# Performance work log

Hardware: AMD Instinct MI355X
Metric: run time of the kernel (lower is better)

## Reference

```python
import jax, jax.numpy as jnp
import numpy as np

N = 50000
IN_CH = 256
HID = 16
HEADS = 4
OUT_CH = 40
E = 800000
NEG_SLOPE = 0.2


def gat_layer(x, src, dst, W, a_src, a_dst, b, heads, out_ch, concat):
    n = x.shape[0]
    h = (x @ W).reshape(n, heads, out_ch)               # [N, H, C]
    al_src = jnp.einsum('nhc,hc->nh', h, a_src)          # [N, H]
    al_dst = jnp.einsum('nhc,hc->nh', h, a_dst)
    e = jax.nn.leaky_relu(al_src[src] + al_dst[dst], NEG_SLOPE)  # [E, H]
    m = jax.ops.segment_max(e, dst, num_segments=n)      # per-dst max for stability
    e = jnp.exp(e - m[dst])
    denom = jax.ops.segment_sum(e, dst, num_segments=n)
    alpha = e / (denom[dst] + 1e-16)                     # segment softmax [E, H]
    msg = h[src] * alpha[:, :, None]                     # [E, H, C]
    out = jax.ops.segment_sum(msg, dst, num_segments=n)  # [N, H, C]
    out = out.reshape(n, heads * out_ch) if concat else out.mean(axis=1)
    return out + b


def setup_inputs() -> dict:
    key = jax.random.key(0)
    ks = jax.random.split(key, 10)
    glorot = lambda k, shape: jax.random.normal(k, shape, jnp.float32) * np.sqrt(2.0 / (shape[0] + shape[-1]))
    return {
        'x': jax.random.normal(ks[0], (N, IN_CH), jnp.float32),
        'edge_index': jax.random.randint(ks[1], (2, E), 0, N, jnp.int64),
        'W1': glorot(ks[2], (IN_CH, HEADS * HID)),
        'a_src1': glorot(ks[3], (HEADS, HID)),
        'a_dst1': glorot(ks[4], (HEADS, HID)),
        'b1': jnp.zeros((HEADS * HID,), jnp.float32),
        'W2': glorot(ks[5], (HEADS * HID, OUT_CH)),
        'a_src2': glorot(ks[6], (1, OUT_CH)),
        'a_dst2': glorot(ks[7], (1, OUT_CH)),
        'b2': jnp.zeros((OUT_CH,), jnp.float32),
    }


def reference(x, edge_index, W1, a_src1, a_dst1, b1, W2, a_src2, a_dst2, b2):
    n = x.shape[0]
    loops = jnp.arange(n, dtype=edge_index.dtype)
    src = jnp.concatenate([edge_index[0], loops])  # PyG GATConv adds self-loops
    dst = jnp.concatenate([edge_index[1], loops])
    h = gat_layer(x, src, dst, W1, a_src1, a_dst1, b1, HEADS, HID, concat=True)
    h = jax.nn.elu(h)
    out = gat_layer(h, src, dst, W2, a_src2, a_dst2, b2, 1, OUT_CH, concat=False)
    return jax.nn.log_softmax(out, axis=-1)
```

## Files before the change

### kernel.cpp

```cpp
#include <hip/hip_runtime.h>
#include <math.h>

static constexpr int IN_CH  = 256;
static constexpr int HD1    = 64;
static constexpr int HEADS  = 4;
static constexpr int OUT_CH = 40;
static constexpr float NEG  = 0.2f;
static constexpr int BSH    = 7;
static constexpr int BRNG   = 128;

typedef __attribute__((ext_vector_type(8))) short bf16x8;
typedef __attribute__((ext_vector_type(4))) short s16x4;
typedef __attribute__((ext_vector_type(4))) float f32x4;

static __device__ __forceinline__ short f2bf(float f) {
    union { float f; unsigned u; } v; v.f = f;
    unsigned r = v.u + 0x7FFFu + ((v.u >> 16) & 1u);
    return (short)(r >> 16);
}
static __device__ __forceinline__ float bf2f(unsigned short u) {
    union { unsigned u; float f; } v; v.u = ((unsigned)u) << 16;
    return v.f;
}

__global__ __launch_bounds__(256) void k_bhist(const int* __restrict__ dst, int* __restrict__ bcnt,
                                               int E, int B, int perBlk) {
    __shared__ int lcnt[4096];
    for (int i = threadIdx.x; i < B; i += 256) lcnt[i] = 0;
    __syncthreads();
    const int s0 = blockIdx.x * perBlk;
    const int s1 = min(s0 + perBlk, E);
    for (int i = s0 + threadIdx.x; i < s1; i += 256)
        atomicAdd(&lcnt[dst[i] >> BSH], 1);
    __syncthreads();
    for (int i = threadIdx.x; i < B; i += 256)
        if (lcnt[i]) atomicAdd(&bcnt[i], lcnt[i]);
}

__global__ __launch_bounds__(256) void k_balloc(const int* __restrict__ bcnt, int* __restrict__ ebstart,
        int* __restrict__ ebcur, int* __restrict__ sstart, int* __restrict__ totals, int B, int n) {
    int t = blockIdx.x * 256 + threadIdx.x;
    if (t < B) {
        int ec = bcnt[t];
        int nodes = min(n - (t << BSH), BRNG);
        ebstart[t] = atomicAdd(&totals[0], ec);
        ebcur[t]   = ebstart[t];
        sstart[t]  = atomicAdd(&totals[1], ec + nodes);
    }
}

__global__ __launch_bounds__(256) void k_bpart(const int* __restrict__ ei, int* __restrict__ ebcur,
        uint2* __restrict__ ebuf, int E, int B, int perBlk) {
    __shared__ int lcnt[4096];
    __shared__ int lofs[4096];
    for (int i = threadIdx.x; i < B; i += 256) lcnt[i] = 0;
    __syncthreads();
    const int s0 = blockIdx.x * perBlk;
    const int s1 = min(s0 + perBlk, E);
    for (int i = s0 + threadIdx.x; i < s1; i += 256)
        atomicAdd(&lcnt[ei[E + i] >> BSH], 1);
    __syncthreads();
    for (int i = threadIdx.x; i < B; i += 256) {
        const int c = lcnt[i];
        lofs[i] = c ? atomicAdd(&ebcur[i], c) : 0;
        lcnt[i] = 0;
    }
    __syncthreads();
    for (int i = s0 + threadIdx.x; i < s1; i += 256) {
        const int d = ei[E + i], s = ei[i];
        const int b = d >> BSH;
        const int r = atomicAdd(&lcnt[b], 1);
        ebuf[lofs[b] + r] = make_uint2((unsigned)s, (unsigned)d);
    }
}

__global__ __launch_bounds__(256) void k_bcsr(const uint2* __restrict__ ebuf,
        const int* __restrict__ ebstart, const int* __restrict__ bcnt, const int* __restrict__ sstart,
        int* __restrict__ rowstart, int* __restrict__ counts, int* __restrict__ ssrc, int n) {
    __shared__ int ncnt[BRNG], rloc[BRNG], cur[BRNG];
    const int b = blockIdx.x;
    const int t = threadIdx.x;
    const int n0 = b << BSH;
    const int nodes = min(n - n0, BRNG);
    const int ec = bcnt[b];
    const int e0 = ebstart[b];
    const int s0 = sstart[b];

    if (t < BRNG) ncnt[t] = (t < nodes) ? 1 : 0;
    __syncthreads();
    for (int i = t; i < ec; i += 256)
        atomicAdd(&ncnt[ebuf[e0 + i].y & (BRNG - 1)], 1);
    __syncthreads();

    if (t < BRNG) rloc[t] = ncnt[t];
    __syncthreads();
    #pragma unroll
    for (int off = 1; off < BRNG; off <<= 1) {
        int u = 0;
        if (t < BRNG && t >= off) u = rloc[t - off];
        __syncthreads();
        if (t < BRNG) rloc[t] += u;
        __syncthreads();
    }

    if (t < nodes) {
        const int ex = rloc[t] - ncnt[t];
        rowstart[n0 + t] = s0 + ex;
        counts[n0 + t]   = ncnt[t];
        ssrc[s0 + ex]    = n0 + t;
        cur[t] = ex + 1;
    }
    __syncthreads();
    for (int i = t; i < ec; i += 256) {
        const uint2 e = ebuf[e0 + i];
        const int lo = (int)e.y & (BRNG - 1);
        const int p = atomicAdd(&cur[lo], 1);
        ssrc[s0 + p] = (int)e.x;
    }
}

__global__ __launch_bounds__(256) void k_xform1(const float* __restrict__ x,
        const float* __restrict__ W1, const float* __restrict__ a_src, const float* __restrict__ a_dst,
        unsigned short* __restrict__ h1b, float* __restrict__ alsrc, float* __restrict__ aldst, int n)
{
    __shared__ short W1T[64][264];
    const int t = threadIdx.x;
    const int l = t & 63;
    const int w = t >> 6;

    {
        const int c = l;
        #pragma unroll
        for (int i = 0; i < 16; ++i) {
            const int kb = i * 16 + w * 4;
            s16x4 pk;
            pk[0] = f2bf(W1[(kb + 0) * 64 + c]);
            pk[1] = f2bf(W1[(kb + 1) * 64 + c]);
            pk[2] = f2bf(W1[(kb + 2) * 64 + c]);
            pk[3] = f2bf(W1[(kb + 3) * 64 + c]);
            *(s16x4*)&W1T[c][kb] = pk;
        }
    }
    __syncthreads();

    const int r0 = blockIdx.x * 64 + w * 16;
    const int lr = l & 15;
    const int lk = l >> 4;

    f32x4 acc[4];
    #pragma unroll
    for (int ct = 0; ct < 4; ++ct) acc[ct] = (f32x4){0.f, 0.f, 0.f, 0.f};

    int rowA = r0 + lr; if (rowA > n - 1) rowA = n - 1;
    const float* xrow = x + (size_t)rowA * IN_CH + lk * 8;

    float4 a0 = *(const float4*)(xrow);
    float4 a1 = *(const float4*)(xrow + 4);

    for (int ks = 0; ks < 8; ++ks) {
        bf16x8 bfrag[4];
        #pragma unroll
        for (int ct = 0; ct < 4; ++ct)
            bfrag[ct] = *(const bf16x8*)&W1T[ct * 16 + lr][ks * 32 + lk * 8];

        const float4 c0 = a0, c1 = a1;
        if (ks < 7) {
            a0 = *(const float4*)(xrow + (ks + 1) * 32);
            a1 = *(const float4*)(xrow + (ks + 1) * 32 + 4);
        }
        bf16x8 afrag;
        afrag[0] = f2bf(c0.x); afrag[1] = f2bf(c0.y);
        afrag[2] = f2bf(c0.z); afrag[3] = f2bf(c0.w);
        afrag[4] = f2bf(c1.x); afrag[5] = f2bf(c1.y);
        afrag[6] = f2bf(c1.z); afrag[7] = f2bf(c1.w);

        #pragma unroll
        for (int ct = 0; ct < 4; ++ct)
            acc[ct] = __builtin_amdgcn_mfma_f32_16x16x32_bf16(afrag, bfrag[ct], acc[ct], 0, 0, 0);
    }

    #pragma unroll
    for (int ct = 0; ct < 4; ++ct) {
        #pragma unroll
        for (int reg = 0; reg < 4; ++reg) {
            const int row = r0 + lk * 4 + reg;
            if (row < n) h1b[(size_t)row * HD1 + ct * 16 + lr] = (unsigned short)f2bf(acc[ct][reg]);
        }
    }

    float asv[4], adv[4];
    #pragma unroll
    for (int ct = 0; ct < 4; ++ct) { asv[ct] = a_src[ct * 16 + lr]; adv[ct] = a_dst[ct * 16 + lr]; }

    #pragma unroll
    for (int reg = 0; reg < 4; ++reg) {
        const int row = r0 + lk * 4 + reg;
        #pragma unroll
        for (int ct = 0; ct < 4; ++ct) {
            float s1 = acc[ct][reg] * asv[ct];
            float s2 = acc[ct][reg] * adv[ct];
            s1 += __shfl_xor(s1, 1); s1 += __shfl_xor(s1, 2);
            s1 += __shfl_xor(s1, 4); s1 += __shfl_xor(s1, 8);
            s2 += __shfl_xor(s2, 1); s2 += __shfl_xor(s2, 2);
            s2 += __shfl_xor(s2, 4); s2 += __shfl_xor(s2, 8);
            if (lr == 0 && row < n) {
                alsrc[row * HEADS + ct] = s1;
                aldst[row * HEADS + ct] = s2;
            }
        }
    }
}

__global__ __launch_bounds__(256) void k_aggr1(const unsigned short* __restrict__ h1b,
        const float* __restrict__ alsrc, const float* __restrict__ aldst, const float* __restrict__ b1,
        const int* __restrict__ rowstart, const int* __restrict__ counts, const int* __restrict__ ssrc,
        float* __restrict__ hact, int n)
{
    const int wid  = (blockIdx.x * blockDim.x + threadIdx.x) >> 6;
    const int lane = threadIdx.x & 63;
    const int sub  = lane & 15;
    const int head = sub >> 2;

    int nid = wid * 4 + (lane >> 4);
    const bool valid = nid < n;
    if (!valid) nid = n - 1;

    const int rs  = rowstart[nid];
    const int cnt = valid ? counts[nid] : 0;

    int maxcnt = cnt;
    maxcnt = max(maxcnt, __shfl_xor(maxcnt, 16));
    maxcnt = max(maxcnt, __shfl_xor(maxcnt, 32));

    float m = -1e30f;
    {
        const float adA = aldst[nid * HEADS + (sub & 3)];
        const int npairs = cnt * 4, maxpairs = maxcnt * 4;
        for (int idx = sub; idx < maxpairs; idx += 16) {
            if (idx < npairs) {
                int s = ssrc[rs + (idx >> 2)];
                float l = alsrc[s * HEADS + (sub & 3)] + adA;
                l = l > 0.f ? l : NEG * l;
                m = fmaxf(m, l);
            }
        }
        #pragma unroll
        for (int off = 1; off < 16; off <<= 1) m = fmaxf(m, __shfl_xor(m, off));
    }

    const float adB = aldst[nid * HEADS + head];
    float d = 0.f;
    float4 acc = make_float4(0.f, 0.f, 0.f, 0.f);
    for (int i0 = 0; i0 < maxcnt; i0 += 4) {
        int  sv[4]; bool on[4];
        #pragma unroll
        for (int u = 0; u < 4; ++u) {
            const int i = i0 + u;
            on[u] = i < cnt;
            sv[u] = on[u] ? ssrc[rs + i] : 0;
        }
        ushort4 hv[4]; float lv[4];
        #pragma unroll
        for (int u = 0; u < 4; ++u) {
            hv[u] = *(const ushort4*)(h1b + (size_t)sv[u] * HD1 + sub * 4);
            lv[u] = alsrc[sv[u] * HEADS + head];
        }
        #pragma unroll
        for (int u = 0; u < 4; ++u) {
            float l = lv[u] + adB;
            l = l > 0.f ? l : NEG * l;
            const float p = on[u] ? __expf(l - m) : 0.f;
            d += p;
            acc.x = fmaf(p, bf2f(hv[u].x), acc.x);
            acc.y = fmaf(p, bf2f(hv[u].y), acc.y);
            acc.z = fmaf(p, bf2f(hv[u].z), acc.z);
            acc.w = fmaf(p, bf2f(hv[u].w), acc.w);
        }
    }

    const float inv = 1.f / (d + 1e-16f);
    const float4 bv = *(const float4*)(b1 + sub * 4);
    float4 v;
    v.x = acc.x * inv + bv.x;  v.y = acc.y * inv + bv.y;
    v.z = acc.z * inv + bv.z;  v.w = acc.w * inv + bv.w;
    v.x = v.x > 0.f ? v.x : __expf(v.x) - 1.f;
    v.y = v.y > 0.f ? v.y : __expf(v.y) - 1.f;
    v.z = v.z > 0.f ? v.z : __expf(v.z) - 1.f;
    v.w = v.w > 0.f ? v.w : __expf(v.w) - 1.f;
    if (valid) *(float4*)(hact + (size_t)nid * HD1 + sub * 4) = v;
}

__global__ __launch_bounds__(64) void k_xform2(const float* __restrict__ hin,
        const float* __restrict__ W2, const float* __restrict__ a_src, const float* __restrict__ a_dst,
        unsigned short* __restrict__ h2b, float* __restrict__ alsrc, float* __restrict__ aldst, int n)
{
    __shared__ float Ws[HD1 * OUT_CH];
    const int t = threadIdx.x;
    #pragma unroll
    for (int i = 0; i < 10; ++i) ((float4*)Ws)[i * 64 + t] = ((const float4*)W2)[i * 64 + t];
    __syncthreads();

    const int r = blockIdx.x * 64 + t;
    if (r >= n) return;

    float acc[OUT_CH];
    #pragma unroll
    for (int j = 0; j < OUT_CH; ++j) acc[j] = 0.f;

    const float4* hr = (const float4*)(hin + (size_t)r * HD1);
    for (int kq = 0; kq < 16; ++kq) {
        const float4 xv = hr[kq];
        #pragma unroll
        for (int kk = 0; kk < 4; ++kk) {
            const float xs = (kk == 0) ? xv.x : (kk == 1) ? xv.y : (kk == 2) ? xv.z : xv.w;
            const float* wrow = Ws + (kq * 4 + kk) * OUT_CH;
            #pragma unroll
            for (int jq = 0; jq < 10; ++jq) {
                const float4 w = *(const float4*)(wrow + jq * 4);
                acc[jq * 4 + 0] = fmaf(xs, w.x, acc[jq * 4 + 0]);
                acc[jq * 4 + 1] = fmaf(xs, w.y, acc[jq * 4 + 1]);
                acc[jq * 4 + 2] = fmaf(xs, w.z, acc[jq * 4 + 2]);
                acc[jq * 4 + 3] = fmaf(xs, w.w, acc[jq * 4 + 3]);
            }
        }
    }

    float s1 = 0.f, s2 = 0.f;
    #pragma unroll
    for (int jq = 0; jq < 10; ++jq) {
        const float4 av = ((const float4*)a_src)[jq];
        const float4 dv = ((const float4*)a_dst)[jq];
        s1 += acc[jq*4+0] * av.x + acc[jq*4+1] * av.y + acc[jq*4+2] * av.z + acc[jq*4+3] * av.w;
        s2 += acc[jq*4+0] * dv.x + acc[jq*4+1] * dv.y + acc[jq*4+2] * dv.z + acc[jq*4+3] * dv.w;
        ushort4 pk;
        pk.x = (unsigned short)f2bf(acc[jq*4+0]);
        pk.y = (unsigned short)f2bf(acc[jq*4+1]);
        pk.z = (unsigned short)f2bf(acc[jq*4+2]);
        pk.w = (unsigned short)f2bf(acc[jq*4+3]);
        *(ushort4*)(h2b + (size_t)r * OUT_CH + jq * 4) = pk;
    }
    alsrc[r] = s1;
    aldst[r] = s2;
}

__global__ __launch_bounds__(256) void k_aggr2(const unsigned short* __restrict__ h2b,
        const float* __restrict__ alsrc, const float* __restrict__ aldst, const float* __restrict__ b2,
        const int* __restrict__ rowstart, const int* __restrict__ counts, const int* __restrict__ ssrc,
        float* __restrict__ out, int n)
{
    const int wid  = (blockIdx.x * blockDim.x + threadIdx.x) >> 6;
    const int lane = threadIdx.x & 63;
    const int sub  = lane & 15;
    const bool act = sub < 10;
    const int subc = act ? sub : 0;

    int nid = wid * 4 + (lane >> 4);
    const bool valid = nid < n;
    if (!valid) nid = n - 1;

    const int rs  = rowstart[nid];
    const int cnt = valid ? counts[nid] : 0;

    int maxcnt = cnt;
    maxcnt = max(maxcnt, __shfl_xor(maxcnt, 16));
    maxcnt = max(maxcnt, __shfl_xor(maxcnt, 32));

    const float ad = aldst[nid];

    float m = -1e30f;
    for (int e = sub; e < maxcnt; e += 16) {
        if (e < cnt) {
            int s = ssrc[rs + e];
            float l = alsrc[s] + ad;
            l = l > 0.f ? l : NEG * l;
            m = fmaxf(m, l);
        }
    }
    #pragma unroll
    for (int off = 1; off < 16; off <<= 1) m = fmaxf(m, __shfl_xor(m, off));

    float d = 0.f;
    float4 acc = make_float4(0.f, 0.f, 0.f, 0.f);
    for (int i0 = 0; i0 < maxcnt; i0 += 4) {
        int  sv[4]; bool on[4];
        #pragma unroll
        for (int u = 0; u < 4; ++u) {
            const int i = i0 + u;
            on[u] = i < cnt;
            sv[u] = on[u] ? ssrc[rs + i] : 0;
        }
        ushort4 hv[4]; float lv[4];
        #pragma unroll
        for (int u = 0; u < 4; ++u) {
            hv[u] = *(const ushort4*)(h2b + (size_t)sv[u] * OUT_CH + subc * 4);
            lv[u] = alsrc[sv[u]];
        }
        #pragma unroll
        for (int u = 0; u < 4; ++u) {
            float l = lv[u] + ad;
            l = l > 0.f ? l : NEG * l;
            const float p = on[u] ? __expf(l - m) : 0.f;
            d += p;
            acc.x = fmaf(p, bf2f(hv[u].x), acc.x);
            acc.y = fmaf(p, bf2f(hv[u].y), acc.y);
            acc.z = fmaf(p, bf2f(hv[u].z), acc.z);
            acc.w = fmaf(p, bf2f(hv[u].w), acc.w);
        }
    }

    const float inv = 1.f / (d + 1e-16f);
    const float4 bv = *(const float4*)(b2 + subc * 4);
    float4 v;
    v.x = acc.x * inv + bv.x;  v.y = acc.y * inv + bv.y;
    v.z = acc.z * inv + bv.z;  v.w = acc.w * inv + bv.w;

    float mv = act ? fmaxf(fmaxf(v.x, v.y), fmaxf(v.z, v.w)) : -1e30f;
    #pragma unroll
    for (int off = 1; off < 16; off <<= 1) mv = fmaxf(mv, __shfl_xor(mv, off));
    float ex = act ? (__expf(v.x - mv) + __expf(v.y - mv) + __expf(v.z - mv) + __expf(v.w - mv)) : 0.f;
    #pragma unroll
    for (int off = 1; off < 16; off <<= 1) ex += __shfl_xor(ex, off);
    const float lse = mv + __logf(ex);

    if (valid && act) {
        *(float4*)(out + (size_t)nid * OUT_CH + sub * 4) =
            make_float4(v.x - lse, v.y - lse, v.z - lse, v.w - lse);
    }
}

extern "C" void kernel_launch(void* const* d_in, const int* in_sizes, int n_in,
                              void* d_out, int out_size, void* d_ws, size_t ws_size,
                              hipStream_t stream) {
    const float* x      = (const float*)d_in[0];
    const int*   ei     = (const int*)d_in[1];
    const float* W1     = (const float*)d_in[2];
    const float* a_src1 = (const float*)d_in[3];
    const float* a_dst1 = (const float*)d_in[4];
    const float* b1     = (const float*)d_in[5];
    const float* W2     = (const float*)d_in[6];
    const float* a_src2 = (const float*)d_in[7];
    const float* a_dst2 = (const float*)d_in[8];
    const float* b2     = (const float*)d_in[9];
    float* out = (float*)d_out;

    const int N = in_sizes[0] / IN_CH;
    const int E = in_sizes[1] / 2;
    const int B = (N + BRNG - 1) >> BSH;

    char* p = (char*)d_ws;
    auto alloc = [&](size_t bytes) -> void* {
        void* r = (void*)p;
        p += (bytes + 255) & ~(size_t)255;
        return r;
    };
    int*   counts   = (int*)alloc((size_t)N * 4);
    int*   rowstart = (int*)alloc((size_t)N * 4);
    int*   ssrc     = (int*)alloc((size_t)(E + N) * 4);
    int*   bmeta    = (int*)alloc((size_t)(B + 2) * 4);
    int*   ebstart  = (int*)alloc((size_t)B * 4);
    int*   ebcur    = (int*)alloc((size_t)B * 4);
    int*   sstart   = (int*)alloc((size_t)B * 4);
    unsigned short* h1b = (unsigned short*)alloc((size_t)N * HD1 * 2);
    unsigned short* h2b = (unsigned short*)alloc((size_t)N * OUT_CH * 2);
    float* alsrc1   = (float*)alloc((size_t)N * HEADS * 4);
    float* aldst1   = (float*)alloc((size_t)N * HEADS * 4);
    float* hact     = (float*)alloc((size_t)N * HD1 * 4);
    uint2* ebuf     = (uint2*)hact;
    int* bcnt   = bmeta;
    int* totals = bmeta + B;
    float* alsrc2 = alsrc1; float* aldst2 = aldst1;

    const int perBlk = 8192;
    const int nblkE  = (E + perBlk - 1) / perBlk;
    const int nblk64 = (N + 63) / 64;
    const int nblkAg = (N + 15) / 16;

    hipMemsetAsync(bmeta, 0, (size_t)(B + 2) * 4, stream);
    k_bhist <<<nblkE, 256, 0, stream>>>(ei + E, bcnt, E, B, perBlk);
    k_balloc<<<(B + 255) / 256, 256, 0, stream>>>(bcnt, ebstart, ebcur, sstart, totals, B, N);
    k_bpart <<<nblkE, 256, 0, stream>>>(ei, ebcur, ebuf, E, B, perBlk);
    k_bcsr  <<<B, 256, 0, stream>>>(ebuf, ebstart, bcnt, sstart, rowstart, counts, ssrc, N);

    k_xform1 <<<nblk64, 256, 0, stream>>>(x, W1, a_src1, a_dst1, h1b, alsrc1, aldst1, N);
    k_aggr1  <<<nblkAg, 256, 0, stream>>>(h1b, alsrc1, aldst1, b1, rowstart, counts, ssrc, hact, N);
    k_xform2 <<<nblk64, 64, 0, stream>>>(hact, W2, a_src2, a_dst2, h2b, alsrc2, aldst2, N);
    k_aggr2  <<<nblkAg, 256, 0, stream>>>(h2b, alsrc2, aldst2, b2, rowstart, counts, ssrc, out, N);
}
```

Before: 148.9 us.

## Replace per-node softmax max pass with global max-based upper bound

Both aggregation kernels stop doing a separate pass over each node's edges to find the per-destination max logit. Instead, the transform kernels reduce a global max of the source attention scores per head (via ordered-uint atomicMax), and the aggregation uses leaky_relu(dst score + global max) as the stabilizer. This relies on softmax being shift-invariant and leaky_relu being monotonic, so it removes a full gather pass over edges. The risk is exp underflow when a node's true max is far below the bound. The hipMemsetAsync call is also replaced by a small zeroing kernel that also clears the max slots.

Result: slower. 160.7 us (+7.9%).

```diff
diff --git a/kernel.cpp b/kernel.cpp
--- a/kernel.cpp
+++ b/kernel.cpp
@@ -21,6 +21,20 @@
 static __device__ __forceinline__ float bf2f(unsigned short u) {
     union { unsigned u; float f; } v; v.u = ((unsigned)u) << 16;
     return v.f;
+}
+static __device__ __forceinline__ unsigned f2ord(float f) {
+    unsigned u = __float_as_uint(f);
+    return (u & 0x80000000u) ? ~u : (u | 0x80000000u);
+}
+static __device__ __forceinline__ float ord2f(unsigned k) {
+    unsigned u = (k & 0x80000000u) ? (k ^ 0x80000000u) : ~k;
+    return __uint_as_float(u);
+}
+
+__global__ __launch_bounds__(256) void k_zero(int* __restrict__ bmeta, unsigned* __restrict__ gmax, int B) {
+    int t = blockIdx.x * 256 + threadIdx.x;
+    if (t < B + 2) bmeta[t] = 0;
+    if (t < 8) gmax[t] = 0u;
 }
 
 __global__ __launch_bounds__(256) void k_bhist(const int* __restrict__ dst, int* __restrict__ bcnt,
@@ -121,9 +135,11 @@
 
 __global__ __launch_bounds__(256) void k_xform1(const float* __restrict__ x,
         const float* __restrict__ W1, const float* __restrict__ a_src, const float* __restrict__ a_dst,
-        unsigned short* __restrict__ h1b, float* __restrict__ alsrc, float* __restrict__ aldst, int n)
+        unsigned short* __restrict__ h1b, float* __restrict__ alsrc, float* __restrict__ aldst,
+        unsigned* __restrict__ gmax, int n)
 {
     __shared__ short W1T[64][264];
+    __shared__ float wmax[4][4];
     const int t = threadIdx.x;
     const int l = t & 63;
     const int w = t >> 6;
@@ -192,6 +208,7 @@
     #pragma unroll
     for (int ct = 0; ct < 4; ++ct) { asv[ct] = a_src[ct * 16 + lr]; adv[ct] = a_dst[ct * 16 + lr]; }
 
+    float mh[4] = {-1e30f, -1e30f, -1e30f, -1e30f};
     #pragma unroll
     for (int reg = 0; reg < 4; ++reg) {
         const int row = r0 + lk * 4 + reg;
@@ -203,18 +220,30 @@
             s1 += __shfl_xor(s1, 4); s1 += __shfl_xor(s1, 8);
             s2 += __shfl_xor(s2, 1); s2 += __shfl_xor(s2, 2);
             s2 += __shfl_xor(s2, 4); s2 += __shfl_xor(s2, 8);
+            mh[ct] = fmaxf(mh[ct], s1);
             if (lr == 0 && row < n) {
                 alsrc[row * HEADS + ct] = s1;
                 aldst[row * HEADS + ct] = s2;
             }
         }
     }
+    #pragma unroll
+    for (int ct = 0; ct < 4; ++ct) {
+        mh[ct] = fmaxf(mh[ct], __shfl_xor(mh[ct], 16));
+        mh[ct] = fmaxf(mh[ct], __shfl_xor(mh[ct], 32));
+    }
+    if (l == 0) { wmax[w][0] = mh[0]; wmax[w][1] = mh[1]; wmax[w][2] = mh[2]; wmax[w][3] = mh[3]; }
+    __syncthreads();
+    if (t < 4) {
+        float m = fmaxf(fmaxf(wmax[0][t], wmax[1][t]), fmaxf(wmax[2][t], wmax[3][t]));
+        atomicMax(&gmax[t], f2ord(m));
+    }
 }
 
 __global__ __launch_bounds__(256) void k_aggr1(const unsigned short* __restrict__ h1b,
         const float* __restrict__ alsrc, const float* __restrict__ aldst, const float* __restrict__ b1,
         const int* __restrict__ rowstart, const int* __restrict__ counts, const int* __restrict__ ssrc,
-        float* __restrict__ hact, int n)
+        const unsigned* __restrict__ gmax, float* __restrict__ hact, int n)
 {
     const int wid  = (blockIdx.x * blockDim.x + threadIdx.x) >> 6;
     const int lane = threadIdx.x & 63;
@@ -232,23 +261,10 @@
     maxcnt = max(maxcnt, __shfl_xor(maxcnt, 16));
     maxcnt = max(maxcnt, __shfl_xor(maxcnt, 32));
 
-    float m = -1e30f;
-    {
-        const float adA = aldst[nid * HEADS + (sub & 3)];
-        const int npairs = cnt * 4, maxpairs = maxcnt * 4;
-        for (int idx = sub; idx < maxpairs; idx += 16) {
-            if (idx < npairs) {
-                int s = ssrc[rs + (idx >> 2)];
-                float l = alsrc[s * HEADS + (sub & 3)] + adA;
-                l = l > 0.f ? l : NEG * l;
-                m = fmaxf(m, l);
-            }
-        }
-        #pragma unroll
-        for (int off = 1; off < 16; off <<= 1) m = fmaxf(m, __shfl_xor(m, off));
-    }
-
     const float adB = aldst[nid * HEADS + head];
+    float m = adB + ord2f(gmax[head]);
+    m = m > 0.f ? m : NEG * m;
+
     float d = 0.f;
     float4 acc = make_float4(0.f, 0.f, 0.f, 0.f);
     for (int i0 = 0; i0 < maxcnt; i0 += 4) {
@@ -292,7 +308,8 @@
 
 __global__ __launch_bounds__(64) void k_xform2(const float* __restrict__ hin,
         const float* __restrict__ W2, const float* __restrict__ a_src, const float* __restrict__ a_dst,
-        unsigned short* __restrict__ h2b, float* __restrict__ alsrc, float* __restrict__ aldst, int n)
+        unsigned short* __restrict__ h2b, float* __restrict__ alsrc, float* __restrict__ aldst,
+        unsigned* __restrict__ gmax, int n)
 {
     __shared__ float Ws[HD1 * OUT_CH];
     const int t = threadIdx.x;
@@ -300,8 +317,9 @@
     for (int i = 0; i < 10; ++i) ((float4*)Ws)[i * 64 + t] = ((const float4*)W2)[i * 64 + t];
     __syncthreads();
 
-    const int r = blockIdx.x * 64 + t;
-    if (r >= n) return;
+    const int r0 = blockIdx.x * 64 + t;
+    const bool valid = r0 < n;
+    const int r = valid ? r0 : n - 1;
 
     float acc[OUT_CH];
     #pragma unroll
@@ -332,21 +350,27 @@
         const float4 dv = ((const float4*)a_dst)[jq];
         s1 += acc[jq*4+0] * av.x + acc[jq*4+1] * av.y + acc[jq*4+2] * av.z + acc[jq*4+3] * av.w;
         s2 += acc[jq*4+0] * dv.x + acc[jq*4+1] * dv.y + acc[jq*4+2] * dv.z + acc[jq*4+3] * dv.w;
-        ushort4 pk;
-        pk.x = (unsigned short)f2bf(acc[jq*4+0]);
-        pk.y = (unsigned short)f2bf(acc[jq*4+1]);
-        pk.z = (unsigned short)f2bf(acc[jq*4+2]);
-        pk.w = (unsigned short)f2bf(acc[jq*4+3]);
-        *(ushort4*)(h2b + (size_t)r * OUT_CH + jq * 4) = pk;
-    }
-    alsrc[r] = s1;
-    aldst[r] = s2;
+        if (valid) {
+            ushort4 pk;
+            pk.x = (unsigned short)f2bf(acc[jq*4+0]);
+            pk.y = (unsigned short)f2bf(acc[jq*4+1]);
+            pk.z = (unsigned short)f2bf(acc[jq*4+2]);
+            pk.w = (unsigned short)f2bf(acc[jq*4+3]);
+            *(ushort4*)(h2b + (size_t)r * OUT_CH + jq * 4) = pk;
+        }
+    }
+    if (valid) { alsrc[r] = s1; aldst[r] = s2; }
+
+    float mred = s1;
+    #pragma unroll
+    for (int off = 1; off < 64; off <<= 1) mred = fmaxf(mred, __shfl_xor(mred, off));
+    if (t == 0) atomicMax(&gmax[4], f2ord(mred));
 }
 
 __global__ __launch_bounds__(256) void k_aggr2(const unsigned short* __restrict__ h2b,
         const float* __restrict__ alsrc, const float* __restrict__ aldst, const float* __restrict__ b2,
         const int* __restrict__ rowstart, const int* __restrict__ counts, const int* __restrict__ ssrc,
-        float* __restrict__ out, int n)
+        const unsigned* __restrict__ gmax, float* __restrict__ out, int n)
 {
     const int wid  = (blockIdx.x * blockDim.x + threadIdx.x) >> 6;
     const int lane = threadIdx.x & 63;
@@ -366,18 +390,8 @@
     maxcnt = max(maxcnt, __shfl_xor(maxcnt, 32));
 
     const float ad = aldst[nid];
-
-    float m = -1e30f;
-    for (int e = sub; e < maxcnt; e += 16) {
-        if (e < cnt) {
-            int s = ssrc[rs + e];
-            float l = alsrc[s] + ad;
-            l = l > 0.f ? l : NEG * l;
-            m = fmaxf(m, l);
-        }
-    }
-    #pragma unroll
-    for (int off = 1; off < 16; off <<= 1) m = fmaxf(m, __shfl_xor(m, off));
+    float m = ad + ord2f(gmax[4]);
+    m = m > 0.f ? m : NEG * m;
 
     float d = 0.f;
     float4 acc = make_float4(0.f, 0.f, 0.f, 0.f);
@@ -460,6 +474,7 @@
     int*   ebstart  = (int*)alloc((size_t)B * 4);
     int*   ebcur    = (int*)alloc((size_t)B * 4);
     int*   sstart   = (int*)alloc((size_t)B * 4);
+    unsigned* gmax  = (unsigned*)alloc(8 * 4);
     unsigned short* h1b = (unsigned short*)alloc((size_t)N * HD1 * 2);
     unsigned short* h2b = (unsigned short*)alloc((size_t)N * OUT_CH * 2);
     float* alsrc1   = (float*)alloc((size_t)N * HEADS * 4);
@@ -475,14 +490,14 @@
     const int nblk64 = (N + 63) / 64;
     const int nblkAg = (N + 15) / 16;
 
-    hipMemsetAsync(bmeta, 0, (size_t)(B + 2) * 4, stream);
+    k_zero  <<<(B + 2 + 255) / 256, 256, 0, stream>>>(bmeta, gmax, B);
     k_bhist <<<nblkE, 256, 0, stream>>>(ei + E, bcnt, E, B, perBlk);
     k_balloc<<<(B + 255) / 256, 256, 0, stream>>>(bcnt, ebstart, ebcur, sstart, totals, B, N);
     k_bpart <<<nblkE, 256, 0, stream>>>(ei, ebcur, ebuf, E, B, perBlk);
     k_bcsr  <<<B, 256, 0, stream>>>(ebuf, ebstart, bcnt, sstart, rowstart, counts, ssrc, N);
 
-    k_xform1 <<<nblk64, 256, 0, stream>>>(x, W1, a_src1, a_dst1, h1b, alsrc1, aldst1, N);
-    k_aggr1  <<<nblkAg, 256, 0, stream>>>(h1b, alsrc1, aldst1, b1, rowstart, counts, ssrc, hact, N);
-    k_xform2 <<<nblk64, 64, 0, stream>>>(hact, W2, a_src2, a_dst2, h2b, alsrc2, aldst2, N);
-    k_aggr2  <<<nblkAg, 256, 0, stream>>>(h2b, alsrc2, aldst2, b2, rowstart, counts, ssrc, out, N);
-}
+    k_xform1 <<<nblk64, 256, 0, stream>>>(x, W1, a_src1, a_dst1, h1b, alsrc1, aldst1, gmax, N);
+    k_aggr1  <<<nblkAg, 256, 0, stream>>>(h1b, alsrc1, aldst1, b1, rowstart, counts, ssrc, gmax, hact, N);
+    k_xform2 <<<nblk64, 64, 0, stream>>>(hact, W2, a_src2, a_dst2, h2b, alsrc2, aldst2, gmax, N);
+    k_aggr2  <<<nblkAg, 256, 0, stream>>>(h2b, alsrc2, aldst2, b2, rowstart, counts, ssrc, gmax, out, N);
+}
```
